# Kernel optimization log

Hardware: AMD Instinct MI355X
Metric: run time of the kernel (lower is better)

The kernel has to match this reference:

```python
import jax, jax.numpy as jnp
import numpy as np

DIM = 512
HEADS = 8
DIM_HEAD = 64  # default dim_head used for scale, matches DIM//HEADS here
SCALE = DIM_HEAD ** -0.5
B, X, Y = 8, 32, 32


def setup_inputs() -> dict:
    key = jax.random.key(0)
    k0, k1, k2, k3 = jax.random.split(key, 4)
    fmap = jax.random.normal(k0, (B, DIM, X, Y), dtype=jnp.float32)
    # 1x1 convs as matrices: weight [out, in]
    Wqkvl = jax.random.normal(k1, (4 * DIM, DIM), dtype=jnp.float32) * (DIM ** -0.5)
    Wout = jax.random.normal(k2, (DIM, DIM), dtype=jnp.float32) * (DIM ** -0.5)
    bout = jax.random.normal(k3, (DIM,), dtype=jnp.float32) * 0.01
    return {"fmap": fmap, "Wqkvl": Wqkvl, "Wout": Wout, "bout": bout}


def reference(fmap, Wqkvl, Wout, bout):
    b, c, x, y = fmap.shape
    h, d = HEADS, c // HEADS
    n = x * y
    # 1x1 conv projection to q,k,v,L
    qkvL = jnp.einsum('oc,bcxy->boxy', Wqkvl, fmap)  # [b, 4c, x, y]
    q, k, v, L = jnp.split(qkvL, 4, axis=1)
    # 'b (h d) x y -> b h (x y) d'
    def to_tokens(t):
        return t.reshape(b, h, d, n).transpose(0, 1, 3, 2)
    q, k, v, L = map(to_tokens, (q, k, v, L))
    dots = jnp.einsum('bhid,bhjd->bhij', q, k) * SCALE  # [b,h,n,n]
    attn = jax.nn.softmax(dots, axis=-1)
    out = jnp.einsum('bhij,bhjd->bhid', attn, v) + L  # [b,h,n,d]
    # 'b h (x y) d -> b (h d) x y'
    out = out.transpose(0, 1, 3, 2).reshape(b, c, x, y)
    # output 1x1 conv with bias (dropout=0 -> identity)
    out = jnp.einsum('oc,bcxy->boxy', Wout, out) + bout[None, :, None, None]
    return out
```

## Files before the change

### kernel.cpp

```cpp
#include <hip/hip_runtime.h>

#define Bn 8
#define Cn 512
#define Hn 8
#define Dn 64
#define Nn 1024
#define SCALEQ 0.18033688011112042f

typedef unsigned short u16;
typedef unsigned short u16x8 __attribute__((ext_vector_type(8)));
typedef unsigned short u16x4 __attribute__((ext_vector_type(4)));
typedef short s16x4 __attribute__((ext_vector_type(4)));
typedef float f32x4 __attribute__((ext_vector_type(4)));
typedef __bf16 bf16x8 __attribute__((ext_vector_type(8)));

__device__ __forceinline__ u16 f2bf(float f){
  unsigned u = __float_as_uint(f);
  u += 0x7fffu + ((u >> 16) & 1u);
  return (u16)(u >> 16);
}
__device__ __forceinline__ float bf2f(u16 h){
  return __uint_as_float(((unsigned)h) << 16);
}
__device__ __forceinline__ f32x4 mfma16(u16x8 a, u16x8 b, f32x4 c){
  return __builtin_amdgcn_mfma_f32_16x16x32_bf16(
      __builtin_bit_cast(bf16x8, a), __builtin_bit_cast(bf16x8, b), c, 0, 0, 0);
}
__device__ __forceinline__ f32x4 mfma16k16(u16x4 a, u16x4 b, f32x4 c){
  return __builtin_amdgcn_mfma_f32_16x16x16bf16_1k(
      __builtin_bit_cast(s16x4, a), __builtin_bit_cast(s16x4, b), c, 0, 0, 0);
}

__device__ __forceinline__ void gload16(const u16* src, u16* dst){
  __builtin_amdgcn_global_load_lds(
      (const __attribute__((address_space(1))) unsigned int*)src,
      (__attribute__((address_space(3))) unsigned int*)dst, 16, 0, 0);
}

__global__ __launch_bounds__(256) void k_convert2(const float* __restrict__ s1,
                                                  const float* __restrict__ s2,
                                                  u16* __restrict__ d1, u16* __restrict__ d2,
                                                  int n1, int n2){
  int i = blockIdx.x * 256 + threadIdx.x;
  const float* s; u16* d; int j;
  if (i < n1){ s = s1; d = d1; j = i; }
  else { if (i >= n1 + n2) return; s = s2; d = d2; j = i - n1; }
  float4 f = reinterpret_cast<const float4*>(s)[j];
  u16x4 o;
  o[0] = f2bf(f.x); o[1] = f2bf(f.y); o[2] = f2bf(f.z); o[3] = f2bf(f.w);
  reinterpret_cast<u16x4*>(d)[j] = o;
}

__global__ __launch_bounds__(256) void k_transpose(const float* __restrict__ fmap,
                                                   u16* __restrict__ fmapT){
  __shared__ float tile[64][33];
  const int n0 = blockIdx.x * 32, c0 = blockIdx.y * 64, b = blockIdx.z;
  const int tx = threadIdx.x & 31, ty = threadIdx.x >> 5;
  const float* src = fmap + ((size_t)b * Cn + c0) * Nn + n0;
#pragma unroll
  for (int i = 0; i < 8; i++) tile[ty + 8*i][tx] = src[(size_t)(ty + 8*i) * Nn + tx];
  __syncthreads();
  const int nr = threadIdx.x >> 3;
  const int cj = (threadIdx.x & 7) * 8;
  u16x8 o;
#pragma unroll
  for (int k = 0; k < 8; k++) o[k] = f2bf(tile[cj + k][nr]);
  *reinterpret_cast<u16x8*>(fmapT + ((size_t)b * Nn + n0 + nr) * Cn + c0 + cj) = o;
}

__device__ __forceinline__ void stageK(const u16* g, u16* lbase, int w, int lane){
#pragma unroll
  for (int s = 0; s < 4; s++){
    int row = s*32 + w*8 + (lane>>3);
    gload16(g + (size_t)row*Cn + (((lane&7) ^ (row&7)) * 8), lbase + (s*32 + w*8)*64);
  }
}
__device__ __forceinline__ void stageV(const u16* g, u16* lbase, int w, int lane){
#pragma unroll
  for (int s = 0; s < 4; s++){
    int row = s*16 + w*4 + (lane>>4);
    gload16(g + (size_t)row*Nn + (((lane&15) ^ (row&7)) * 8), lbase + (s*16 + w*4)*128);
  }
}
__device__ __forceinline__ void stage128x32(const u16* g, size_t ldg, u16* lbase, int w, int lane){
#pragma unroll
  for (int s = 0; s < 2; s++){
    int row = s*64 + w*16 + (lane>>2);
    gload16(g + (size_t)row*ldg + (((lane&3) ^ (row&3)) * 8), lbase + (s*64 + w*16)*32);
  }
}
__device__ __forceinline__ void stage64x32(const u16* g, size_t ldg, u16* lbase, int w, int lane){
  int row = w*16 + (lane>>2);
  gload16(g + (size_t)row*ldg + (((lane&3) ^ (row&3)) * 8), lbase + (w*16)*32);
}

__device__ __forceinline__ void gemm_fma(const u16x8 (&af)[4], const u16x8 (&bf)[4],
                                         f32x4 (&acc)[4][4]){
#pragma unroll
  for (int i = 0; i < 4; i++)
#pragma unroll
    for (int j = 0; j < 4; j++)
      acc[i][j] = mfma16(af[i], bf[j], acc[i][j]);
}

__device__ __forceinline__ void gemm_nt_128(const u16* __restrict__ Ap, int lda,
                                            const u16* __restrict__ Bp, int ldb,
                                            u16* sA, u16* sB,
                                            f32x4 (&acc)[4][4]){
  const int tid = threadIdx.x;
  const int w = tid >> 6, lane = tid & 63, r = lane & 15, g = lane >> 4;
  const int wi = w >> 1, wj = w & 1;
  stage128x32(Ap, lda, sA, w, lane);
  stage128x32(Bp, ldb, sB, w, lane);
  for (int ks = 0; ks < Cn/32; ks++){
    __syncthreads();
    const int cur = ks & 1;
    if (ks + 1 < Cn/32){
      stage128x32(Ap + (ks+1)*32, lda, sA + (cur^1)*128*32, w, lane);
      stage128x32(Bp + (ks+1)*32, ldb, sB + (cur^1)*128*32, w, lane);
    }
    const u16* Al = sA + cur*128*32;
    const u16* Bl = sB + cur*128*32;
    u16x8 af[4], bf[4];
#pragma unroll
    for (int t = 0; t < 4; t++){
      int ar = wi*64 + t*16 + r;
      af[t] = *reinterpret_cast<const u16x8*>(&Al[ar*32 + ((g ^ (ar&3)) * 8)]);
      int br = wj*64 + t*16 + r;
      bf[t] = *reinterpret_cast<const u16x8*>(&Bl[br*32 + ((g ^ (br&3)) * 8)]);
    }
    gemm_fma(af, bf, acc);
  }
}

__global__ __launch_bounds__(256) void k_gemm1(const u16* __restrict__ fmapT,
                                               const u16* __restrict__ W1,
                                               u16* __restrict__ Qb, u16* __restrict__ Kb,
                                               u16* __restrict__ Vt, u16* __restrict__ Lb){
  __shared__ u16 sA[2*128*32], sB[2*128*32];
  const int lin = blockIdx.x;
  const int wid = (lin & 7) * 128 + (lin >> 3);
  const int ob = wid & 15, nb = (wid >> 4) & 7, b = wid >> 7;
  const int w = threadIdx.x >> 6, wi = w >> 1, wj = w & 1;
  const int lane = threadIdx.x & 63, r = lane & 15, g = lane >> 4;
  const int seg = ob >> 2;

  f32x4 acc[4][4];
  const f32x4 z = {0.f, 0.f, 0.f, 0.f};
#pragma unroll
  for (int i = 0; i < 4; i++)
#pragma unroll
    for (int j = 0; j < 4; j++) acc[i][j] = z;

  const u16* fbase = fmapT + (size_t)b * Nn * Cn;

  if (seg != 2){
    gemm_nt_128(fbase + (size_t)(nb*128) * Cn, Cn, W1 + (size_t)(ob*128) * Cn, Cn, sA, sB, acc);
    u16* dst = (seg == 0) ? Qb : (seg == 1 ? Kb : Lb);
    const float sc = (seg == 0) ? SCALEQ : 1.0f;
#pragma unroll
    for (int it = 0; it < 4; it++)
#pragma unroll
      for (int jt = 0; jt < 4; jt++)
#pragma unroll
        for (int rr = 0; rr < 4; rr++){
          int n = nb*128 + wi*64 + it*16 + 4*g + rr;
          int o = ob*128 + wj*64 + jt*16 + r;
          dst[((size_t)b * Nn + n) * Cn + (o & 511)] = f2bf(acc[it][jt][rr] * sc);
        }
  } else {
    gemm_nt_128(W1 + (size_t)(ob*128) * Cn, Cn, fbase + (size_t)(nb*128) * Cn, Cn, sA, sB, acc);
#pragma unroll
    for (int it = 0; it < 4; it++)
#pragma unroll
      for (int jt = 0; jt < 4; jt++)
#pragma unroll
        for (int rr = 0; rr < 4; rr++){
          int o = ob*128 + wi*64 + it*16 + 4*g + rr;
          int oo = o - 1024;
          int h = oo >> 6, d = oo & 63;
          int n = nb*128 + wj*64 + jt*16 + r;
          Vt[(((size_t)b * Hn + h) * Dn + d) * Nn + n] = f2bf(acc[it][jt][rr]);
        }
  }
}

__device__ __forceinline__ void attn_tile(const u16* Kc, const u16* Vc,
                                          const u16* kbase, const u16* vbase, int next,
                                          u16* Kn, u16* Vn,
                                          int w, int lane, int r, int g,
                                          u16x8 qA0, u16x8 qA1, u16x8 qB0, u16x8 qB1,
                                          f32x4 (&accA)[4], f32x4 (&accB)[4],
                                          f32x4& accSA, f32x4& accSB){
  const f32x4 z = {0.f, 0.f, 0.f, 0.f};
  __syncthreads();
  if (next < 8){
    stageK(kbase + (size_t)next*128*Cn, Kn, w, lane);
    stageV(vbase + next*128,            Vn, w, lane);
  }
  f32x4 sA[8], sB[8];
#pragma unroll
  for (int t = 0; t < 8; t++){
    int row = 16*t + r;
    u16x8 k0 = *reinterpret_cast<const u16x8*>(&Kc[row*64 + ((g     ^ (r&7)) * 8)]);
    u16x8 k1 = *reinterpret_cast<const u16x8*>(&Kc[row*64 + (((4+g) ^ (r&7)) * 8)]);
    sA[t] = mfma16(k0, qA0, z); sA[t] = mfma16(k1, qA1, sA[t]);
    sB[t] = mfma16(k0, qB0, z); sB[t] = mfma16(k1, qB1, sB[t]);
  }
  u16x4 pA[8], pB[8];
#pragma unroll
  for (int t = 0; t < 8; t++){
#pragma unroll
    for (int j = 0; j < 4; j++){
      pA[t][j] = __builtin_bit_cast(u16, (__bf16)exp2f(sA[t][j]));
      pB[t][j] = __builtin_bit_cast(u16, (__bf16)exp2f(sB[t][j]));
    }
  }
  const u16x4 ones = {0x3F80u, 0x3F80u, 0x3F80u, 0x3F80u};
#pragma unroll
  for (int t = 0; t < 8; t++){
    accSA = mfma16k16(ones, pA[t], accSA);
    accSB = mfma16k16(ones, pB[t], accSB);
  }
#pragma unroll
  for (int s = 0; s < 8; s++)
#pragma unroll
    for (int dt = 0; dt < 4; dt++){
      int row = dt*16 + r;
      u16x4 vf = *reinterpret_cast<const u16x4*>(
          &Vc[row*128 + (((2*s + (g>>1)) ^ (r&7)) * 8) + (g&1)*4]);
      accA[dt] = mfma16k16(vf, pA[s], accA[dt]);
      accB[dt] = mfma16k16(vf, pB[s], accB[dt]);
    }
}

__global__ __launch_bounds__(256, 2) void k_attn(const u16* __restrict__ Qb,
                                                 const u16* __restrict__ Kb,
                                                 const u16* __restrict__ Vt,
                                                 const u16* __restrict__ Lb,
                                                 u16* __restrict__ tok){
  __shared__ u16 Kl[2*128*64], Vl[2*64*128];
  const int bid = blockIdx.x;
  const int w0 = (bid & 7) * 64 + (bid >> 3);
  const int qblk = w0 & 7, h = (w0 >> 3) & 7, b = w0 >> 6;
  const int w = threadIdx.x >> 6, lane = threadIdx.x & 63;
  const int r = lane & 15, g = lane >> 4;
  const int qA = qblk * 128 + w * 16;
  const int qB = qA + 64;

  const u16* qrowA = Qb + ((size_t)b * Nn + qA + r) * Cn + h * Dn + 8 * g;
  const u16* qrowB = Qb + ((size_t)b * Nn + qB + r) * Cn + h * Dn + 8 * g;
  u16x8 qA0 = *reinterpret_cast<const u16x8*>(qrowA);
  u16x8 qA1 = *reinterpret_cast<const u16x8*>(qrowA + 32);
  u16x8 qB0 = *reinterpret_cast<const u16x8*>(qrowB);
  u16x8 qB1 = *reinterpret_cast<const u16x8*>(qrowB + 32);

  const u16* kbase = Kb + (size_t)b * Nn * Cn + h * Dn;
  const u16* vbase = Vt + ((size_t)b * Hn + h) * Dn * Nn;

  f32x4 accA[4], accB[4];
  const f32x4 z = {0.f, 0.f, 0.f, 0.f};
#pragma unroll
  for (int dt = 0; dt < 4; dt++){ accA[dt] = z; accB[dt] = z; }
  f32x4 accSA = z, accSB = z;

  u16* Kl0 = Kl, *Kl1 = Kl + 128*64;
  u16* Vl0 = Vl, *Vl1 = Vl + 64*128;
  stageK(kbase, Kl0, w, lane);
  stageV(vbase, Vl0, w, lane);

  for (int tile = 0; tile < 8; tile += 2){
    attn_tile(Kl0, Vl0, kbase, vbase, tile + 1, Kl1, Vl1, w, lane, r, g,
              qA0, qA1, qB0, qB1, accA, accB, accSA, accSB);
    attn_tile(Kl1, Vl1, kbase, vbase, tile + 2, Kl0, Vl0, w, lane, r, g,
              qA0, qA1, qB0, qB1, accA, accB, accSA, accSB);
  }

  float linvA = 1.0f / accSA[0];
  float linvB = 1.0f / accSB[0];
#pragma unroll
  for (int half = 0; half < 2; half++){
    const int n = (half ? qB : qA) + r;
    const float linv = half ? linvB : linvA;
    const f32x4* acc = half ? accB : accA;
    const u16* lrow = Lb + ((size_t)b * Nn + n) * Cn + h * Dn;
    u16* trow = tok + ((size_t)b * Nn + n) * Cn + h * Dn;
#pragma unroll
    for (int dt = 0; dt < 4; dt++){
      u16x4 lv = *reinterpret_cast<const u16x4*>(lrow + dt*16 + 4*g);
      u16x4 ov;
#pragma unroll
      for (int rr = 0; rr < 4; rr++)
        ov[rr] = f2bf(acc[dt][rr] * linv + bf2f(lv[rr]));
      *reinterpret_cast<u16x4*>(trow + dt*16 + 4*g) = ov;
    }
  }
}

__global__ __launch_bounds__(256) void k_gemm2(const u16* __restrict__ tok,
                                               const u16* __restrict__ Wo,
                                               const float* __restrict__ bout,
                                               float* __restrict__ out){
  __shared__ u16 sA[2*64*32], sB[2*128*32];
  const int lin = blockIdx.x;
  const int wid = (lin & 7) * 64 + (lin >> 3);
  const int ob = wid & 7, nb = (wid >> 3) & 7, b = wid >> 6;
  const int w = threadIdx.x >> 6, wi = w >> 1, wj = w & 1;
  const int lane = threadIdx.x & 63, r = lane & 15, g = lane >> 4;

  f32x4 acc[2][4];
  const f32x4 z = {0.f, 0.f, 0.f, 0.f};
#pragma unroll
  for (int i = 0; i < 2; i++)
#pragma unroll
    for (int j = 0; j < 4; j++) acc[i][j] = z;

  const u16* Ap = Wo + (size_t)(ob*64) * Cn;
  const u16* Bp = tok + (size_t)b * Nn * Cn + (size_t)(nb*128) * Cn;

  stage64x32(Ap, Cn, sA, w, lane);
  stage128x32(Bp, Cn, sB, w, lane);
  for (int ks = 0; ks < Cn/32; ks++){
    __syncthreads();
    const int cur = ks & 1;
    if (ks + 1 < Cn/32){
      stage64x32(Ap + (ks+1)*32, Cn, sA + (cur^1)*64*32, w, lane);
      stage128x32(Bp + (ks+1)*32, Cn, sB + (cur^1)*128*32, w, lane);
    }
    const u16* Al = sA + cur*64*32;
    const u16* Bl = sB + cur*128*32;
    u16x8 af[2], bf[4];
#pragma unroll
    for (int t = 0; t < 2; t++){
      int ar = wi*32 + t*16 + r;
      af[t] = *reinterpret_cast<const u16x8*>(&Al[ar*32 + ((g ^ (ar&3)) * 8)]);
    }
#pragma unroll
    for (int t = 0; t < 4; t++){
      int br = wj*64 + t*16 + r;
      bf[t] = *reinterpret_cast<const u16x8*>(&Bl[br*32 + ((g ^ (br&3)) * 8)]);
    }
#pragma unroll
    for (int i = 0; i < 2; i++)
#pragma unroll
      for (int j = 0; j < 4; j++)
        acc[i][j] = mfma16(af[i], bf[j], acc[i][j]);
  }

#pragma unroll
  for (int it = 0; it < 2; it++)
#pragma unroll
    for (int jt = 0; jt < 4; jt++)
#pragma unroll
      for (int rr = 0; rr < 4; rr++){
        int o = ob*64 + wi*32 + it*16 + 4*g + rr;
        int n = nb*128 + wj*64 + jt*16 + r;
        out[((size_t)b * Cn + o) * Nn + n] = acc[it][jt][rr] + bout[o];
      }
}

extern "C" void kernel_launch(void* const* d_in, const int* in_sizes, int n_in,
                              void* d_out, int out_size, void* d_ws, size_t ws_size,
                              hipStream_t stream){
  const float* fmap  = (const float*)d_in[0];
  const float* Wqkvl = (const float*)d_in[1];
  const float* Wout  = (const float*)d_in[2];
  const float* bout  = (const float*)d_in[3];
  float* out = (float*)d_out;

  char* ws = (char*)d_ws;
  size_t off = 0;
  auto alloc = [&](size_t bytes) -> void* {
    void* p = ws + off;
    off += (bytes + 255) & ~(size_t)255;
    return p;
  };
  u16* W1bf  = (u16*)alloc((size_t)4*Cn*Cn*2);
  u16* Wobf  = (u16*)alloc((size_t)Cn*Cn*2);
  u16* fmapT = (u16*)alloc((size_t)Bn*Nn*Cn*2);
  u16* Qb    = (u16*)alloc((size_t)Bn*Nn*Cn*2);
  u16* Kb    = (u16*)alloc((size_t)Bn*Nn*Cn*2);
  u16* Lb    = (u16*)alloc((size_t)Bn*Nn*Cn*2);
  u16* Vt    = (u16*)alloc((size_t)Bn*Hn*Dn*Nn*2);
  u16* tok   = fmapT;

  const int n1 = 4*Cn*Cn/4, n2 = Cn*Cn/4;
  hipLaunchKernelGGL(k_convert2, dim3((n1 + n2 + 255)/256), dim3(256), 0, stream,
                     Wqkvl, Wout, W1bf, Wobf, n1, n2);
  hipLaunchKernelGGL(k_transpose, dim3(Nn/32, Cn/64, Bn), dim3(256), 0, stream, fmap, fmapT);
  hipLaunchKernelGGL(k_gemm1, dim3(1024), dim3(256), 0, stream, fmapT, W1bf, Qb, Kb, Vt, Lb);
  hipLaunchKernelGGL(k_attn, dim3(512), dim3(256), 0, stream, Qb, Kb, Vt, Lb, tok);
  hipLaunchKernelGGL(k_gemm2, dim3(512), dim3(256), 0, stream, tok, Wobf, bout, out);
}
```

Baseline: 92.04 us.

## Split attention block into 8 waves of 16 queries with 64-key tiles

The attention kernel moves from 4 waves each handling two 16-row query groups to 8 waves each handling one 16-row group, keeping 128 queries per block. The key/value tiles shrink from 128 to 64 keys, doubling the number of loop iterations and barriers while halving shared memory per block. Per-wave register pressure drops (one accumulator set instead of two), and launch bounds rise to 512 threads with 4 blocks, aiming for more waves in flight to hide latency. The cost is twice as many syncs and LDS fragment loads per useful MFMA, since each K/V fragment read now feeds only one query group.

After: 92.32 us. About the same (+0.3%).

```diff
diff --git a/kernel.cpp b/kernel.cpp
--- a/kernel.cpp
+++ b/kernel.cpp
@@ -68,19 +68,9 @@
   *reinterpret_cast<u16x8*>(fmapT + ((size_t)b * Nn + n0 + nr) * Cn + c0 + cj) = o;
 }
 
-__device__ __forceinline__ void stageK(const u16* g, u16* lbase, int w, int lane){
-#pragma unroll
-  for (int s = 0; s < 4; s++){
-    int row = s*32 + w*8 + (lane>>3);
-    gload16(g + (size_t)row*Cn + (((lane&7) ^ (row&7)) * 8), lbase + (s*32 + w*8)*64);
-  }
-}
-__device__ __forceinline__ void stageV(const u16* g, u16* lbase, int w, int lane){
-#pragma unroll
-  for (int s = 0; s < 4; s++){
-    int row = s*16 + w*4 + (lane>>4);
-    gload16(g + (size_t)row*Nn + (((lane&15) ^ (row&7)) * 8), lbase + (s*16 + w*4)*128);
-  }
+__device__ __forceinline__ void stage64_8w(const u16* g, size_t ldg, u16* lbase, int w, int lane){
+  int row = w*8 + (lane>>3);
+  gload16(g + (size_t)row*ldg + (((lane&7) ^ (row&7)) * 8), lbase + (w*8)*64);
 }
 __device__ __forceinline__ void stage128x32(const u16* g, size_t ldg, u16* lbase, int w, int lane){
 #pragma unroll
@@ -189,111 +179,93 @@
                                           const u16* kbase, const u16* vbase, int next,
                                           u16* Kn, u16* Vn,
                                           int w, int lane, int r, int g,
-                                          u16x8 qA0, u16x8 qA1, u16x8 qB0, u16x8 qB1,
-                                          f32x4 (&accA)[4], f32x4 (&accB)[4],
-                                          f32x4& accSA, f32x4& accSB){
+                                          u16x8 qf0, u16x8 qf1,
+                                          f32x4 (&accO)[4], f32x4& accS){
   const f32x4 z = {0.f, 0.f, 0.f, 0.f};
   __syncthreads();
-  if (next < 8){
-    stageK(kbase + (size_t)next*128*Cn, Kn, w, lane);
-    stageV(vbase + next*128,            Vn, w, lane);
-  }
-  f32x4 sA[8], sB[8];
-#pragma unroll
-  for (int t = 0; t < 8; t++){
+  if (next < 16){
+    stage64_8w(kbase + (size_t)next*64*Cn, Cn, Kn, w, lane);
+    stage64_8w(vbase + next*64,            Nn, Vn, w, lane);
+  }
+  f32x4 st[4];
+#pragma unroll
+  for (int t = 0; t < 4; t++){
     int row = 16*t + r;
     u16x8 k0 = *reinterpret_cast<const u16x8*>(&Kc[row*64 + ((g     ^ (r&7)) * 8)]);
     u16x8 k1 = *reinterpret_cast<const u16x8*>(&Kc[row*64 + (((4+g) ^ (r&7)) * 8)]);
-    sA[t] = mfma16(k0, qA0, z); sA[t] = mfma16(k1, qA1, sA[t]);
-    sB[t] = mfma16(k0, qB0, z); sB[t] = mfma16(k1, qB1, sB[t]);
-  }
-  u16x4 pA[8], pB[8];
-#pragma unroll
-  for (int t = 0; t < 8; t++){
-#pragma unroll
-    for (int j = 0; j < 4; j++){
-      pA[t][j] = __builtin_bit_cast(u16, (__bf16)exp2f(sA[t][j]));
-      pB[t][j] = __builtin_bit_cast(u16, (__bf16)exp2f(sB[t][j]));
-    }
-  }
+    st[t] = mfma16(k0, qf0, z);
+    st[t] = mfma16(k1, qf1, st[t]);
+  }
+  u16x4 p[4];
+#pragma unroll
+  for (int t = 0; t < 4; t++)
+#pragma unroll
+    for (int j = 0; j < 4; j++)
+      p[t][j] = __builtin_bit_cast(u16, (__bf16)exp2f(st[t][j]));
   const u16x4 ones = {0x3F80u, 0x3F80u, 0x3F80u, 0x3F80u};
 #pragma unroll
-  for (int t = 0; t < 8; t++){
-    accSA = mfma16k16(ones, pA[t], accSA);
-    accSB = mfma16k16(ones, pB[t], accSB);
-  }
-#pragma unroll
-  for (int s = 0; s < 8; s++)
+  for (int t = 0; t < 4; t++) accS = mfma16k16(ones, p[t], accS);
+#pragma unroll
+  for (int s = 0; s < 4; s++)
 #pragma unroll
     for (int dt = 0; dt < 4; dt++){
       int row = dt*16 + r;
       u16x4 vf = *reinterpret_cast<const u16x4*>(
-          &Vc[row*128 + (((2*s + (g>>1)) ^ (r&7)) * 8) + (g&1)*4]);
-      accA[dt] = mfma16k16(vf, pA[s], accA[dt]);
-      accB[dt] = mfma16k16(vf, pB[s], accB[dt]);
-    }
-}
-
-__global__ __launch_bounds__(256, 2) void k_attn(const u16* __restrict__ Qb,
+          &Vc[row*64 + (((2*s + (g>>1)) ^ (r&7)) * 8) + (g&1)*4]);
+      accO[dt] = mfma16k16(vf, p[s], accO[dt]);
+    }
+}
+
+__global__ __launch_bounds__(512, 4) void k_attn(const u16* __restrict__ Qb,
                                                  const u16* __restrict__ Kb,
                                                  const u16* __restrict__ Vt,
                                                  const u16* __restrict__ Lb,
                                                  u16* __restrict__ tok){
-  __shared__ u16 Kl[2*128*64], Vl[2*64*128];
+  __shared__ u16 Kl[2*64*64], Vl[2*64*64];
   const int bid = blockIdx.x;
   const int w0 = (bid & 7) * 64 + (bid >> 3);
   const int qblk = w0 & 7, h = (w0 >> 3) & 7, b = w0 >> 6;
   const int w = threadIdx.x >> 6, lane = threadIdx.x & 63;
   const int r = lane & 15, g = lane >> 4;
-  const int qA = qblk * 128 + w * 16;
-  const int qB = qA + 64;
-
-  const u16* qrowA = Qb + ((size_t)b * Nn + qA + r) * Cn + h * Dn + 8 * g;
-  const u16* qrowB = Qb + ((size_t)b * Nn + qB + r) * Cn + h * Dn + 8 * g;
-  u16x8 qA0 = *reinterpret_cast<const u16x8*>(qrowA);
-  u16x8 qA1 = *reinterpret_cast<const u16x8*>(qrowA + 32);
-  u16x8 qB0 = *reinterpret_cast<const u16x8*>(qrowB);
-  u16x8 qB1 = *reinterpret_cast<const u16x8*>(qrowB + 32);
+  const int q0 = qblk * 128 + w * 16;
+
+  const u16* qrow = Qb + ((size_t)b * Nn + q0 + r) * Cn + h * Dn + 8 * g;
+  u16x8 qf0 = *reinterpret_cast<const u16x8*>(qrow);
+  u16x8 qf1 = *reinterpret_cast<const u16x8*>(qrow + 32);
 
   const u16* kbase = Kb + (size_t)b * Nn * Cn + h * Dn;
   const u16* vbase = Vt + ((size_t)b * Hn + h) * Dn * Nn;
 
-  f32x4 accA[4], accB[4];
+  f32x4 accO[4];
   const f32x4 z = {0.f, 0.f, 0.f, 0.f};
 #pragma unroll
-  for (int dt = 0; dt < 4; dt++){ accA[dt] = z; accB[dt] = z; }
-  f32x4 accSA = z, accSB = z;
-
-  u16* Kl0 = Kl, *Kl1 = Kl + 128*64;
-  u16* Vl0 = Vl, *Vl1 = Vl + 64*128;
-  stageK(kbase, Kl0, w, lane);
-  stageV(vbase, Vl0, w, lane);
-
-  for (int tile = 0; tile < 8; tile += 2){
+  for (int dt = 0; dt < 4; dt++) accO[dt] = z;
+  f32x4 accS = z;
+
+  u16* Kl0 = Kl, *Kl1 = Kl + 64*64;
+  u16* Vl0 = Vl, *Vl1 = Vl + 64*64;
+  stage64_8w(kbase, Cn, Kl0, w, lane);
+  stage64_8w(vbase, Nn, Vl0, w, lane);
+
+  for (int tile = 0; tile < 16; tile += 2){
     attn_tile(Kl0, Vl0, kbase, vbase, tile + 1, Kl1, Vl1, w, lane, r, g,
-              qA0, qA1, qB0, qB1, accA, accB, accSA, accSB);
+              qf0, qf1, accO, accS);
     attn_tile(Kl1, Vl1, kbase, vbase, tile + 2, Kl0, Vl0, w, lane, r, g,
-              qA0, qA1, qB0, qB1, accA, accB, accSA, accSB);
-  }
-
-  float linvA = 1.0f / accSA[0];
-  float linvB = 1.0f / accSB[0];
-#pragma unroll
-  for (int half = 0; half < 2; half++){
-    const int n = (half ? qB : qA) + r;
-    const float linv = half ? linvB : linvA;
-    const f32x4* acc = half ? accB : accA;
-    const u16* lrow = Lb + ((size_t)b * Nn + n) * Cn + h * Dn;
-    u16* trow = tok + ((size_t)b * Nn + n) * Cn + h * Dn;
-#pragma unroll
-    for (int dt = 0; dt < 4; dt++){
-      u16x4 lv = *reinterpret_cast<const u16x4*>(lrow + dt*16 + 4*g);
-      u16x4 ov;
-#pragma unroll
-      for (int rr = 0; rr < 4; rr++)
-        ov[rr] = f2bf(acc[dt][rr] * linv + bf2f(lv[rr]));
-      *reinterpret_cast<u16x4*>(trow + dt*16 + 4*g) = ov;
-    }
+              qf0, qf1, accO, accS);
+  }
+
+  float linv = 1.0f / accS[0];
+  const int n = q0 + r;
+  const u16* lrow = Lb + ((size_t)b * Nn + n) * Cn + h * Dn;
+  u16* trow = tok + ((size_t)b * Nn + n) * Cn + h * Dn;
+#pragma unroll
+  for (int dt = 0; dt < 4; dt++){
+    u16x4 lv = *reinterpret_cast<const u16x4*>(lrow + dt*16 + 4*g);
+    u16x4 ov;
+#pragma unroll
+    for (int rr = 0; rr < 4; rr++)
+      ov[rr] = f2bf(accO[dt][rr] * linv + bf2f(lv[rr]));
+    *reinterpret_cast<u16x4*>(trow + dt*16 + 4*g) = ov;
   }
 }
 
@@ -389,6 +361,6 @@
                      Wqkvl, Wout, W1bf, Wobf, n1, n2);
   hipLaunchKernelGGL(k_transpose, dim3(Nn/32, Cn/64, Bn), dim3(256), 0, stream, fmap, fmapT);
   hipLaunchKernelGGL(k_gemm1, dim3(1024), dim3(256), 0, stream, fmapT, W1bf, Qb, Kb, Vt, Lb);
-  hipLaunchKernelGGL(k_attn, dim3(512), dim3(256), 0, stream, Qb, Kb, Vt, Lb, tok);
+  hipLaunchKernelGGL(k_attn, dim3(512), dim3(512), 0, stream, Qb, Kb, Vt, Lb, tok);
   hipLaunchKernelGGL(k_gemm2, dim3(512), dim3(256), 0, stream, tok, Wobf, bout, out);
 }
```
